# Optimization experiments

Hardware: AMD Instinct MI355X
Metric: run time of the kernel (lower is better)

The kernel has to match this reference:

```python
import jax, jax.numpy as jnp
import numpy as np


def setup_inputs() -> dict:
    key = jax.random.key(0)
    k1, k2, k3, k4, k5, k6 = jax.random.split(key, 6)
    B, V = 128, 128000
    logits = jax.random.normal(k1, (B, V), dtype=jnp.float32) * 2.0
    # keep temperatures away from 0 to avoid overflow in logits/temp
    temperatures = 0.7 + 0.6 * jax.random.uniform(k2, (B,), dtype=jnp.float32)
    top_ks = jax.random.randint(k3, (B,), 1, 1024, dtype=jnp.int32)
    top_ps = 0.7 + 0.29 * jax.random.uniform(k4, (B,), dtype=jnp.float32)
    min_ps = 0.02 * jax.random.uniform(k5, (B,), dtype=jnp.float32)
    # uniform variate for inverse-CDF multinomial sampling (one sample per row)
    u = jax.random.uniform(k6, (B, 1), dtype=jnp.float32)
    return {
        "logits": logits,
        "temperatures": temperatures,
        "top_ks": top_ks,
        "top_ps": top_ps,
        "min_ps": min_ps,
        "u": u,
    }


def reference(logits, temperatures, top_ks, top_ps, min_ps, u):
    """Faithful jax version of Sampler's torch-native sampling path:
    softmax(logits/T) -> descending sort -> top-k mask -> top-p mask
    (cumsum computed pre-mask, exactly as torch code) -> min-p mask ->
    multinomial sample (inverse CDF with provided uniform u) ->
    gather original token index. Also returns the renormalized filtered
    probs scattered back to vocab order (top_p_normalize_probs-style)."""
    B, V = logits.shape
    probs = jax.nn.softmax(logits / temperatures[:, None], axis=-1)  # [B, V]

    order = jnp.argsort(-probs, axis=-1)                     # descending indices
    probs_sort = jnp.take_along_axis(probs, order, axis=-1)  # [B, V] sorted desc
    probs_sum = jnp.cumsum(probs_sort, axis=-1)              # cumsum BEFORE masking

    pos = jnp.arange(V, dtype=jnp.int32)[None, :]
    # top-k: zero everything at rank >= top_k
    probs_sort = jnp.where(pos >= top_ks[:, None], 0.0, probs_sort)
    # top-p: zero where cumulative mass strictly before this token exceeds top_p
    probs_sort = jnp.where(probs_sum - probs_sort > top_ps[:, None], 0.0, probs_sort)
    # min-p: threshold relative to the max prob (rank-0 entry survives both masks)
    min_p_thr = probs_sort[:, :1] * min_ps[:, None]
    probs_sort = jnp.where(probs_sort < min_p_thr, 0.0, probs_sort)

    total = jnp.sum(probs_sort, axis=-1, keepdims=True)      # [B, 1]
    cdf = jnp.cumsum(probs_sort, axis=-1) / total            # normalized CDF
    # inverse-CDF sampling == torch.multinomial(probs_sort, 1)
    sampled_rank = jnp.clip(jnp.sum(cdf < u, axis=-1, keepdims=True), 0, V - 1)
    token_ids = jnp.take_along_axis(order, sampled_rank, axis=-1)[:, 0].astype(jnp.int32)

    # scatter renormalized filtered probs back to original vocab positions
    inv_order = jnp.argsort(order, axis=-1)
    norm_probs = jnp.take_along_axis(probs_sort / total, inv_order, axis=-1)
    return token_ids, norm_probs
```

## Files before the change

### kernel.cpp

```cpp
#include <hip/hip_runtime.h>
#include <stdint.h>
#include <math.h>

#define TPB 1024
#define NB 2048
#define SPLIT 4
#define LCAND 2560
#define CAND2 2048
#define PS 4096
#define L2E 1.44269504088896f

typedef float vfloat4 __attribute__((ext_vector_type(4)));
typedef unsigned long long ull;

__device__ __forceinline__ unsigned fkey(float f) {
    unsigned u = __float_as_uint(f);
    return (u & 0x80000000u) ? ~u : (u | 0x80000000u);
}
__device__ __forceinline__ float funkey(unsigned k) {
    unsigned u = (k & 0x80000000u) ? (k ^ 0x80000000u) : ~k;
    return __uint_as_float(u);
}
__device__ __forceinline__ ull packkv(unsigned k, unsigned idx) {
    return ((ull)k << 32) | (ull)(~idx);
}

__device__ __forceinline__ void suffix_scan_2048(unsigned* h, unsigned* wscr, int tid)
{
    const int lane = tid & 63, w = tid >> 6;
    const int i0 = 2047 - 2 * tid;
    const int i1 = 2046 - 2 * tid;
    unsigned a = h[i0], b = h[i1];
    unsigned s = a + b;
    unsigned inc = s;
    #pragma unroll
    for (int d = 1; d < 64; d <<= 1) { unsigned o = __shfl_up(inc, d); if (lane >= d) inc += o; }
    if (lane == 63) wscr[w] = inc;
    __syncthreads();
    if (w == 0) {
        unsigned v = (lane < 16) ? wscr[lane] : 0u;
        unsigned vi = v;
        #pragma unroll
        for (int d = 1; d < 16; d <<= 1) { unsigned o = __shfl_up(vi, d); if (lane >= d) vi += o; }
        if (lane < 16) wscr[16 + lane] = vi - v;
    }
    __syncthreads();
    unsigned off = wscr[16 + w] + (inc - s);
    h[i0] = off + a;
    h[i1] = off + a + b;
    __syncthreads();
}

__global__ __launch_bounds__(TPB)
void k1_scan(const float* __restrict__ logits,
             const float* __restrict__ temps,
             const int* __restrict__ top_ks,
             float* __restrict__ out_probs,
             float* __restrict__ ws_meta,
             unsigned* __restrict__ ws_cut,
             unsigned* __restrict__ ws_cnt,
             ull* __restrict__ ws_cand,
             int V, int Vq, int n)
{
    const int blk = blockIdx.x;
    const int tid = threadIdx.x, lane = tid & 63, w = tid >> 6;
    const int role = blk % 3;

    if (role != 0) {
        const int ZB = (gridDim.x / 3) * 2;
        const int zid = (blk / 3) * 2 + (role - 1);
        const int n4 = n >> 2;
        vfloat4* p4 = (vfloat4*)out_probs;
        const vfloat4 z4 = (vfloat4)0.0f;
        const int step = ZB * TPB;
        for (int i = zid * TPB + tid; i < n4; i += step) p4[i] = z4;
        for (int i = (n4 << 2) + zid * TPB + tid; i < n; i += step) out_probs[i] = 0.0f;
        return;
    }

    const int sblk = blk / 3;
    const int b = sblk / SPLIT, s = sblk % SPLIT;
    const int start = s * Vq;
    const int len = min(Vq, V - start);
    const int slot = sblk;
    const float invT = 1.0f / temps[b];
    int K = top_ks[b]; K = max(K, 1); K = min(K, 1024);

    __shared__ unsigned hist[NB];
    __shared__ unsigned uscr[32];
    __shared__ float fred[32];
    __shared__ unsigned cnt;
    __shared__ int bstar;

    if (len <= 0) {
        if (tid == 0) {
            ws_meta[4*slot] = -1e30f; ws_meta[4*slot+1] = 0.0f;
            ws_meta[4*slot+2] = -1e30f; ws_meta[4*slot+3] = __uint_as_float(0u);
            ws_cut[slot] = 0u; ws_cnt[slot] = 0u;
        }
        return;
    }

    for (int i = tid; i < NB; i += TPB) hist[i] = 0;
    if (tid == 0) { cnt = 0; bstar = 0; }
    __syncthreads();

    const float* __restrict__ row = logits + (size_t)b * V + start;
    const vfloat4* __restrict__ row4 = (const vfloat4*)row;
    const int L4 = len >> 2;

    const int nps = min(len, PS);
    float m0 = -1e30f;
    for (int i = tid; i < nps; i += TPB) {
        float lv = row[i];
        m0 = fmaxf(m0, lv);
        atomicAdd(&hist[fkey(lv) >> 21], 1u);
    }
    #pragma unroll
    for (int d = 32; d > 0; d >>= 1) m0 = fmaxf(m0, __shfl_down(m0, d));
    if (lane == 0) fred[w] = m0;
    __syncthreads();
    if (tid == 0) {
        float mm = fred[0];
        for (int j = 1; j < 16; ++j) mm = fmaxf(mm, fred[j]);
        fred[16] = mm;
    }
    __syncthreads();
    const float m0max = fred[16];

    suffix_scan_2048(hist, uscr, tid);
    float sexp = (float)K * (float)nps / (float)V;
    unsigned TGT = (unsigned)(sexp + 6.0f * sqrtf(sexp) + 16.5f);
    if (TGT > (unsigned)nps) TGT = (unsigned)nps;
    for (int e = tid; e < NB; e += TPB) {
        unsigned Se = hist[e];
        unsigned Sn = (e < NB - 1) ? hist[e + 1] : 0u;
        if (Se >= TGT && Sn < TGT) bstar = e;
    }
    __syncthreads();
    const unsigned cutkey = (unsigned)bstar << 21;
    const float cutval = funkey(cutkey);

    const float ca = invT * L2E;
    const float cb = -m0max * invT * L2E;

    float z = 0.0f, mb = -1e30f;
    ull* gc = ws_cand + (size_t)slot * LCAND;

    for (int i = tid; i < L4; i += TPB) {
        vfloat4 v = row4[i];
        float x0 = v[0], x1 = v[1], x2 = v[2], x3 = v[3];
        z += exp2f(fmaf(x0, ca, cb)) + exp2f(fmaf(x1, ca, cb))
           + exp2f(fmaf(x2, ca, cb)) + exp2f(fmaf(x3, ca, cb));
        mb = fmaxf(mb, fmaxf(fmaxf(x0, x1), fmaxf(x2, x3)));
        bool c0 = x0 >= cutval, c1 = x1 >= cutval, c2 = x2 >= cutval, c3 = x3 >= cutval;
        if (c0 | c1 | c2 | c3) {
            int nh = (int)c0 + (int)c1 + (int)c2 + (int)c3;
            unsigned base = atomicAdd(&cnt, (unsigned)nh);
            unsigned bi = (unsigned)(start + (i << 2));
            if (c0) { if (base < LCAND) gc[base] = packkv(fkey(x0), bi + 0); base++; }
            if (c1) { if (base < LCAND) gc[base] = packkv(fkey(x1), bi + 1); base++; }
            if (c2) { if (base < LCAND) gc[base] = packkv(fkey(x2), bi + 2); base++; }
            if (c3) { if (base < LCAND) gc[base] = packkv(fkey(x3), bi + 3); base++; }
        }
    }
    for (int i = (L4 << 2) + tid; i < len; i += TPB) {
        float lv = row[i];
        z += exp2f(fmaf(lv, ca, cb));
        mb = fmaxf(mb, lv);
        if (lv >= cutval) {
            unsigned base = atomicAdd(&cnt, 1u);
            if (base < LCAND) gc[base] = packkv(fkey(lv), (unsigned)(start + i));
        }
    }
    __syncthreads();
    #pragma unroll
    for (int d = 32; d > 0; d >>= 1) {
        z += __shfl_down(z, d);
        mb = fmaxf(mb, __shfl_down(mb, d));
    }
    if (lane == 0) { fred[w] = z; fred[16 + w] = mb; }
    __syncthreads();
    if (tid == 0) {
        float zz = 0.0f, mm = -1e30f;
        for (int j = 0; j < 16; ++j) { zz += fred[j]; mm = fmaxf(mm, fred[16 + j]); }
        ws_meta[4*slot + 0] = m0max * invT;
        ws_meta[4*slot + 1] = zz;
        ws_meta[4*slot + 2] = mm * invT;
        ws_meta[4*slot + 3] = __uint_as_float(fkey(mm));
        ws_cut[slot] = cutkey;
        ws_cnt[slot] = cnt;
    }
}

__global__ __launch_bounds__(TPB)
void k2_sample(const float* __restrict__ logits,
               const float* __restrict__ temps,
               const int* __restrict__ top_ks,
               const float* __restrict__ top_ps,
               const float* __restrict__ min_ps,
               const float* __restrict__ uvec,
               const float* __restrict__ ws_meta,
               const unsigned* __restrict__ ws_cut,
               const unsigned* __restrict__ ws_cnt,
               const ull* __restrict__ ws_cand,
               float* __restrict__ out_tok,
               float* __restrict__ out_probs,
               int V)
{
    const int b = blockIdx.x;
    const int tid = threadIdx.x, lane = tid & 63, w = tid >> 6;
    const float invT = 1.0f / temps[b];
    int Korig = top_ks[b]; Korig = max(Korig, 1); Korig = min(Korig, 1024);
    const unsigned Ku = (unsigned)Korig;
    const float top_p = top_ps[b], min_p = min_ps[b], uval = uvec[b];

    __shared__ __align__(16) char smem[53504];
    ull*            cand  = (ull*)(smem);
    ull*            cand2 = (ull*)(smem + 16384);
    unsigned*       hist  = (unsigned*)(smem + 32768);
    unsigned short* cnts  = (unsigned short*)(smem + 41216);
    float*          sh_p  = (float*)(smem + 45312);
    float*          sh_c  = (float*)(smem + 49408);
    __shared__ unsigned uscr[32];
    __shared__ float fws[32];
    __shared__ unsigned scnt;
    __shared__ int sh_i1, sh_i2;
    __shared__ unsigned sh_u1;

    float Cy[SPLIT], zq[SPLIT], Mbyq[SPLIT];
    unsigned cutq[SPLIT], cntq[SPLIT], mkq[SPLIT];
    #pragma unroll
    for (int q = 0; q < SPLIT; ++q) {
        int sl = b * SPLIT + q;
        Cy[q] = ws_meta[4*sl]; zq[q] = ws_meta[4*sl+1]; Mbyq[q] = ws_meta[4*sl+2];
        mkq[q] = __float_as_uint(ws_meta[4*sl+3]);
        cutq[q] = ws_cut[sl]; cntq[q] = ws_cnt[sl];
    }
    float Y = -1e30f;
    #pragma unroll
    for (int q = 0; q < SPLIT; ++q) Y = fmaxf(Y, Cy[q]);
    float Z = 0.0f;
    #pragma unroll
    for (int q = 0; q < SPLIT; ++q)
        if (zq[q] > 0.0f) Z += zq[q] * exp2f((Cy[q] - Y) * L2E);

    bool fb = false;
    unsigned cutmax = 0, mincut = 0xFFFFFFFFu, maxkey = 0;
    #pragma unroll
    for (int q = 0; q < SPLIT; ++q) {
        if (cntq[q] > (unsigned)LCAND) fb = true;
        if (cntq[q] > 0u) {
            if (Mbyq[q] - Cy[q] > 60.0f) fb = true;
            cutmax = max(cutmax, cutq[q]);
            mincut = min(mincut, cutq[q]);
            maxkey = max(maxkey, mkq[q]);
        }
    }
    if (mincut == 0xFFFFFFFFu) fb = true;

    const unsigned base = mincut;
    const unsigned range = maxkey - base;
    int shift = 0;
    while ((range >> shift) > (unsigned)(NB - 1)) shift++;

    unsigned Tkeyb = 0;
    int count = 0, bstar = 0;

    if (!fb) {
        for (int i = tid; i <= NB; i += TPB) hist[i] = 0;
        if (tid == 0) { sh_i1 = -1; scnt = 0; }
        __syncthreads();
        #pragma unroll
        for (int q = 0; q < SPLIT; ++q) {
            const ull* gc = ws_cand + (size_t)(b * SPLIT + q) * LCAND;
            int nl = min((int)cntq[q], LCAND);
            for (int i = tid; i < nl; i += TPB)
                atomicAdd(&hist[((unsigned)(gc[i] >> 32) - base) >> shift], 1u);
        }
        __syncthreads();
        unsigned fat = 0;
        for (int i = tid; i < NB; i += TPB) {
            unsigned h = hist[i];
            cnts[i] = (unsigned short)h;
            fat = max(fat, h);
        }
        #pragma unroll
        for (int d = 32; d > 0; d >>= 1) fat = max(fat, __shfl_down(fat, d));
        if (lane == 0) uscr[w] = fat;
        __syncthreads();
        if (tid == 0) {
            unsigned m2 = 0;
            for (int j = 0; j < 16; ++j) m2 = max(m2, uscr[j]);
            uscr[16] = m2;
        }
        __syncthreads();
        if (uscr[16] > 64u) fb = true;
    }
    if (!fb) {
        suffix_scan_2048(hist, uscr, tid);
        for (int e = tid; e < NB; e += TPB) {
            unsigned Se = hist[e], Sn = (e < NB - 1) ? hist[e + 1] : 0u;
            if (Se >= Ku && Sn < Ku) { sh_i1 = e; sh_u1 = Se; }
        }
        __syncthreads();
        if (sh_i1 < 0) fb = true;
        else {
            bstar = sh_i1;
            count = (int)sh_u1;
            Tkeyb = base + ((unsigned)bstar << shift);
            if (Tkeyb < cutmax || count > CAND2) fb = true;
        }
    }
    if (!fb) {
        #pragma unroll
        for (int q = 0; q < SPLIT; ++q) {
            const ull* gc = ws_cand + (size_t)(b * SPLIT + q) * LCAND;
            int nl = min((int)cntq[q], LCAND);
            for (int i = tid; i < nl; i += TPB) {
                ull e = gc[i];
                unsigned k = (unsigned)(e >> 32);
                if (k >= Tkeyb) {
                    unsigned bin = (k - base) >> shift;
                    unsigned pos = atomicAdd(&hist[bin + 1], 1u);
                    cand2[pos] = e;
                }
            }
        }
        __syncthreads();
        for (int e = bstar + tid; e < NB; e += TPB) {
            int c = (int)cnts[e];
            if (c >= 2) {
                int st = (int)hist[e + 1] - c;
                for (int x = 1; x < c; ++x) {
                    ull key = cand2[st + x];
                    int y = x - 1;
                    while (y >= 0 && cand2[st + y] < key) { cand2[st + y + 1] = cand2[st + y]; --y; }
                    cand2[st + y + 1] = key;
                }
            }
        }
        __syncthreads();
    }

    if (fb) {
        const float* __restrict__ row = logits + (size_t)b * V;
        float m = -1e30f, z = 0.0f;
        for (int i = tid; i < V; i += TPB) {
            float y = row[i] * invT;
            float nm = fmaxf(m, y);
            z = z * exp2f((m - nm) * L2E) + exp2f((y - nm) * L2E);
            m = nm;
        }
        sh_p[tid] = m; sh_c[tid] = z;
        __syncthreads();
        for (int d = TPB >> 1; d > 0; d >>= 1) {
            if (tid < d) {
                float m1 = sh_p[tid], z1 = sh_c[tid];
                float m2 = sh_p[tid + d], z2 = sh_c[tid + d];
                float mm = fmaxf(m1, m2);
                sh_c[tid] = z1 * exp2f((m1 - mm) * L2E) + z2 * exp2f((m2 - mm) * L2E);
                sh_p[tid] = mm;
            }
            __syncthreads();
        }
        Y = sh_p[0]; Z = sh_c[0];
        __syncthreads();
        for (int i = tid; i < NB; i += TPB) hist[i] = 0;
        if (tid == 0) { sh_i1 = 0; sh_i2 = 0; sh_u1 = 0; }
        __syncthreads();
        for (int i = tid; i < V; i += TPB) atomicAdd(&hist[fkey(row[i]) >> 21], 1u);
        __syncthreads();
        suffix_scan_2048(hist, uscr, tid);
        for (int e = tid; e < NB; e += TPB) {
            unsigned Se = hist[e], Sn = (e < NB-1) ? hist[e+1] : 0u;
            if (Se >= Ku && Sn < Ku) { sh_i1 = e; sh_u1 = Sn; }
        }
        __syncthreads();
        int b1 = sh_i1;
        unsigned cab = sh_u1;
        for (int i = tid; i < NB; i += TPB) hist[i] = 0;
        __syncthreads();
        for (int i = tid; i < V; i += TPB) {
            unsigned k = fkey(row[i]);
            if ((int)(k >> 21) == b1) atomicAdd(&hist[(k >> 10) & (NB - 1)], 1u);
        }
        __syncthreads();
        suffix_scan_2048(hist, uscr, tid);
        for (int e = tid; e < NB; e += TPB) {
            unsigned Se = cab + hist[e];
            unsigned Sn = cab + ((e < NB-1) ? hist[e+1] : 0u);
            if (Se >= Ku && Sn < Ku) sh_i2 = e;
        }
        __syncthreads();
        unsigned Tkey = ((unsigned)b1 << 21) | ((unsigned)sh_i2 << 10);
        if (tid == 0) scnt = 0;
        __syncthreads();
        for (int i = tid; i < V; i += TPB) {
            unsigned k = fkey(row[i]);
            if (k >= Tkey) {
                unsigned pos = atomicAdd(&scnt, 1u);
                if (pos < CAND2) cand[pos] = packkv(k, (unsigned)i);
            }
        }
        __syncthreads();
        count = (scnt < (unsigned)CAND2) ? (int)scnt : CAND2;

        int n_sort = 1;
        while (n_sort < count) n_sort <<= 1;
        for (int i = tid; i < n_sort; i += TPB)
            if (i >= count) cand[i] = 0ull;
        __syncthreads();
        for (int kk = 2; kk <= n_sort; kk <<= 1) {
            for (int j = kk >> 1; j > 0; j >>= 1) {
                for (int i = tid; i < n_sort; i += TPB) {
                    int ixj = i ^ j;
                    if (ixj > i) {
                        ull a = cand[i], c = cand[ixj];
                        bool up = (i & kk) == 0;
                        if (up ? (a < c) : (a > c)) { cand[i] = c; cand[ixj] = a; }
                    }
                }
                __syncthreads();
            }
        }
    }

    ull* srt = fb ? cand : cand2;
    int K = min(Korig, count);

    float pv = 0.0f;
    if (tid < K) {
        unsigned k = (unsigned)(srt[tid] >> 32);
        pv = exp2f((funkey(k) * invT - Y) * L2E) / Z;
    }
    float inc = pv;
    #pragma unroll
    for (int d = 1; d < 64; d <<= 1) { float o = __shfl_up(inc, d); if (lane >= d) inc += o; }
    if (lane == 63) fws[w] = inc;
    __syncthreads();
    if (w == 0) {
        float v = (lane < 16) ? fws[lane] : 0.0f;
        float vi = v;
        #pragma unroll
        for (int d = 1; d < 16; d <<= 1) { float o = __shfl_up(vi, d); if (lane >= d) vi += o; }
        if (lane < 16) fws[16 + lane] = vi - v;
    }
    __syncthreads();
    float cum = inc + fws[16 + w];
    sh_p[tid] = pv;
    sh_c[tid] = cum;
    if (tid == 0) sh_i1 = K;
    __syncthreads();

    if (tid < K) {
        float excl = cum - pv;
        if (excl > top_p) atomicMin(&sh_i1, tid);
    }
    __syncthreads();
    int n1 = sh_i1;
    float thr = sh_p[0] * min_p;
    if (tid == 0) sh_i2 = n1;
    __syncthreads();
    if (tid < n1 && sh_p[tid] < thr) atomicMin(&sh_i2, tid);
    __syncthreads();
    int nf = sh_i2;
    float total = sh_c[nf - 1];

    int pred = (tid < nf) && ((sh_c[tid] / total) < uval);
    int rank = __syncthreads_count(pred);
    if (rank > nf - 1) rank = nf - 1;
    if (rank < 0) rank = 0;
    if (tid == 0)
        out_tok[b] = (float)(~(unsigned)(srt[rank] & 0xFFFFFFFFull));

    if (tid < nf) {
        unsigned idx = ~(unsigned)(srt[tid] & 0xFFFFFFFFull);
        out_probs[(size_t)b * V + idx] = sh_p[tid] / total;
    }
}

extern "C" void kernel_launch(void* const* d_in, const int* in_sizes, int n_in,
                              void* d_out, int out_size, void* d_ws, size_t ws_size,
                              hipStream_t stream) {
    const float* logits = (const float*)d_in[0];
    const float* temps  = (const float*)d_in[1];
    const int*   top_ks = (const int*)d_in[2];
    const float* top_ps = (const float*)d_in[3];
    const float* min_ps = (const float*)d_in[4];
    const float* u      = (const float*)d_in[5];
    const int B = in_sizes[1];
    const int V = in_sizes[0] / B;
    float* out_tok   = (float*)d_out;
    float* out_probs = out_tok + B;

    int Vq = (((V + SPLIT - 1) / SPLIT) + 3) & ~3;
    int n = B * V;

    char* ws = (char*)d_ws;
    size_t off = 0;
    auto take = [&](size_t bytes) { char* p = ws + off; off = (off + bytes + 255) & ~(size_t)255; return p; };
    float*    ws_meta = (float*)take((size_t)B * SPLIT * 4 * sizeof(float));
    unsigned* ws_cut  = (unsigned*)take((size_t)B * SPLIT * sizeof(unsigned));
    unsigned* ws_cnt  = (unsigned*)take((size_t)B * SPLIT * sizeof(unsigned));
    ull*      ws_cand = (ull*)take((size_t)B * SPLIT * LCAND * sizeof(ull));
    (void)ws_size;

    k1_scan<<<dim3(3 * SPLIT * B), dim3(TPB), 0, stream>>>(
        logits, temps, top_ks, out_probs, ws_meta, ws_cut, ws_cnt, ws_cand, V, Vq, n);
    k2_sample<<<dim3(B), dim3(TPB), 0, stream>>>(
        logits, temps, top_ks, top_ps, min_ps, u, ws_meta, ws_cut, ws_cnt, ws_cand,
        out_tok, out_probs, V);
}
```

Measured before the change: 155.5 us.

## Fuse output zeroing into scan blocks, unroll main loop, compute max key from candidates

Removes the separate zero-filling block roles from k1 and has each scan block zero its own slice of the output with nontemporal stores, shrinking the grid threefold. The main pass over the logits is unrolled by four with independent partial sums. The per-slice running max is dropped from that loop; k2 instead recomputes the max key by scanning the candidate lists. The fallback test changes from a max-minus-prefix-max bound to finiteness checks on Z. This trades more parallel blocks for less loop overhead per element, and moves some reduction work into k2.

```diff
diff --git a/kernel.cpp b/kernel.cpp
--- a/kernel.cpp
+++ b/kernel.cpp
@@ -60,26 +60,11 @@
              unsigned* __restrict__ ws_cut,
              unsigned* __restrict__ ws_cnt,
              ull* __restrict__ ws_cand,
-             int V, int Vq, int n)
+             int V, int Vq)
 {
-    const int blk = blockIdx.x;
+    const int sblk = blockIdx.x;
+    const int b = sblk / SPLIT, s = sblk % SPLIT;
     const int tid = threadIdx.x, lane = tid & 63, w = tid >> 6;
-    const int role = blk % 3;
-
-    if (role != 0) {
-        const int ZB = (gridDim.x / 3) * 2;
-        const int zid = (blk / 3) * 2 + (role - 1);
-        const int n4 = n >> 2;
-        vfloat4* p4 = (vfloat4*)out_probs;
-        const vfloat4 z4 = (vfloat4)0.0f;
-        const int step = ZB * TPB;
-        for (int i = zid * TPB + tid; i < n4; i += step) p4[i] = z4;
-        for (int i = (n4 << 2) + zid * TPB + tid; i < n; i += step) out_probs[i] = 0.0f;
-        return;
-    }
-
-    const int sblk = blk / 3;
-    const int b = sblk / SPLIT, s = sblk % SPLIT;
     const int start = s * Vq;
     const int len = min(Vq, V - start);
     const int slot = sblk;
@@ -94,9 +79,8 @@
 
     if (len <= 0) {
         if (tid == 0) {
-            ws_meta[4*slot] = -1e30f; ws_meta[4*slot+1] = 0.0f;
-            ws_meta[4*slot+2] = -1e30f; ws_meta[4*slot+3] = __uint_as_float(0u);
-            ws_cut[slot] = 0u; ws_cnt[slot] = 0u;
+            ws_meta[2*slot] = -1e30f; ws_meta[2*slot+1] = 0.0f;
+            ws_cut[slot] = 0xFFFFFFFFu; ws_cnt[slot] = 0u;
         }
         return;
     }
@@ -141,53 +125,72 @@
     const unsigned cutkey = (unsigned)bstar << 21;
     const float cutval = funkey(cutkey);
 
+    {
+        float* __restrict__ orow = out_probs + (size_t)b * V + start;
+        vfloat4* __restrict__ orow4 = (vfloat4*)orow;
+        const vfloat4 z4 = (vfloat4)0.0f;
+        for (int i = tid; i < L4; i += TPB) __builtin_nontemporal_store(z4, &orow4[i]);
+        for (int i = (L4 << 2) + tid; i < len; i += TPB) __builtin_nontemporal_store(0.0f, &orow[i]);
+    }
+
     const float ca = invT * L2E;
     const float cb = -m0max * invT * L2E;
-
-    float z = 0.0f, mb = -1e30f;
     ull* gc = ws_cand + (size_t)slot * LCAND;
 
-    for (int i = tid; i < L4; i += TPB) {
+    float z0 = 0.0f, z1 = 0.0f, z2 = 0.0f, z3 = 0.0f;
+
+    #define E4(v) (exp2f(fmaf((v)[0], ca, cb)) + exp2f(fmaf((v)[1], ca, cb)) \
+                 + exp2f(fmaf((v)[2], ca, cb)) + exp2f(fmaf((v)[3], ca, cb)))
+    #define GATHER(v, ii) do {                                                  \
+        bool c0 = (v)[0] >= cutval, c1 = (v)[1] >= cutval,                      \
+             c2 = (v)[2] >= cutval, c3 = (v)[3] >= cutval;                      \
+        if (c0 | c1 | c2 | c3) {                                                \
+            int nh = (int)c0 + (int)c1 + (int)c2 + (int)c3;                     \
+            unsigned base = atomicAdd(&cnt, (unsigned)nh);                      \
+            unsigned bi = (unsigned)(start + ((ii) << 2));                      \
+            if (c0) { if (base < LCAND) gc[base] = packkv(fkey((v)[0]), bi+0); base++; } \
+            if (c1) { if (base < LCAND) gc[base] = packkv(fkey((v)[1]), bi+1); base++; } \
+            if (c2) { if (base < LCAND) gc[base] = packkv(fkey((v)[2]), bi+2); base++; } \
+            if (c3) { if (base < LCAND) gc[base] = packkv(fkey((v)[3]), bi+3); base++; } \
+        }                                                                       \
+    } while (0)
+
+    int i = tid;
+    for (; i + 3 * TPB < L4; i += 4 * TPB) {
+        vfloat4 va = row4[i];
+        vfloat4 vb = row4[i + TPB];
+        vfloat4 vc = row4[i + 2 * TPB];
+        vfloat4 vd = row4[i + 3 * TPB];
+        z0 += E4(va); z1 += E4(vb); z2 += E4(vc); z3 += E4(vd);
+        GATHER(va, i); GATHER(vb, i + TPB); GATHER(vc, i + 2 * TPB); GATHER(vd, i + 3 * TPB);
+    }
+    for (; i < L4; i += TPB) {
         vfloat4 v = row4[i];
-        float x0 = v[0], x1 = v[1], x2 = v[2], x3 = v[3];
-        z += exp2f(fmaf(x0, ca, cb)) + exp2f(fmaf(x1, ca, cb))
-           + exp2f(fmaf(x2, ca, cb)) + exp2f(fmaf(x3, ca, cb));
-        mb = fmaxf(mb, fmaxf(fmaxf(x0, x1), fmaxf(x2, x3)));
-        bool c0 = x0 >= cutval, c1 = x1 >= cutval, c2 = x2 >= cutval, c3 = x3 >= cutval;
-        if (c0 | c1 | c2 | c3) {
-            int nh = (int)c0 + (int)c1 + (int)c2 + (int)c3;
-            unsigned base = atomicAdd(&cnt, (unsigned)nh);
-            unsigned bi = (unsigned)(start + (i << 2));
-            if (c0) { if (base < LCAND) gc[base] = packkv(fkey(x0), bi + 0); base++; }
-            if (c1) { if (base < LCAND) gc[base] = packkv(fkey(x1), bi + 1); base++; }
-            if (c2) { if (base < LCAND) gc[base] = packkv(fkey(x2), bi + 2); base++; }
-            if (c3) { if (base < LCAND) gc[base] = packkv(fkey(x3), bi + 3); base++; }
-        }
-    }
-    for (int i = (L4 << 2) + tid; i < len; i += TPB) {
-        float lv = row[i];
-        z += exp2f(fmaf(lv, ca, cb));
-        mb = fmaxf(mb, lv);
+        z0 += E4(v);
+        GATHER(v, i);
+    }
+    for (int j = (L4 << 2) + tid; j < len; j += TPB) {
+        float lv = row[j];
+        z0 += exp2f(fmaf(lv, ca, cb));
         if (lv >= cutval) {
             unsigned base = atomicAdd(&cnt, 1u);
-            if (base < LCAND) gc[base] = packkv(fkey(lv), (unsigned)(start + i));
-        }
-    }
-    __syncthreads();
-    #pragma unroll
-    for (int d = 32; d > 0; d >>= 1) {
-        z += __shfl_down(z, d);
-        mb = fmaxf(mb, __shfl_down(mb, d));
-    }
-    if (lane == 0) { fred[w] = z; fred[16 + w] = mb; }
+            if (base < LCAND) gc[base] = packkv(fkey(lv), (unsigned)(start + j));
+        }
+    }
+    #undef E4
+    #undef GATHER
+
+    float z = (z0 + z1) + (z2 + z3);
+    __syncthreads();
+    #pragma unroll
+    for (int d = 32; d > 0; d >>= 1) z += __shfl_down(z, d);
+    if (lane == 0) fred[w] = z;
     __syncthreads();
     if (tid == 0) {
-        float zz = 0.0f, mm = -1e30f;
-        for (int j = 0; j < 16; ++j) { zz += fred[j]; mm = fmaxf(mm, fred[16 + j]); }
-        ws_meta[4*slot + 0] = m0max * invT;
-        ws_meta[4*slot + 1] = zz;
-        ws_meta[4*slot + 2] = mm * invT;
-        ws_meta[4*slot + 3] = __uint_as_float(fkey(mm));
+        float zz = 0.0f;
+        for (int j = 0; j < 16; ++j) zz += fred[j];
+        ws_meta[2*slot + 0] = m0max * invT;
+        ws_meta[2*slot + 1] = zz;
         ws_cut[slot] = cutkey;
         ws_cnt[slot] = cnt;
     }
@@ -224,53 +227,64 @@
     float*          sh_c  = (float*)(smem + 49408);
     __shared__ unsigned uscr[32];
     __shared__ float fws[32];
-    __shared__ unsigned scnt;
+    __shared__ unsigned scnt, sh_mk;
     __shared__ int sh_i1, sh_i2;
     __shared__ unsigned sh_u1;
 
-    float Cy[SPLIT], zq[SPLIT], Mbyq[SPLIT];
-    unsigned cutq[SPLIT], cntq[SPLIT], mkq[SPLIT];
+    float Cy[SPLIT], zq[SPLIT];
+    unsigned cutq[SPLIT], cntq[SPLIT];
     #pragma unroll
     for (int q = 0; q < SPLIT; ++q) {
         int sl = b * SPLIT + q;
-        Cy[q] = ws_meta[4*sl]; zq[q] = ws_meta[4*sl+1]; Mbyq[q] = ws_meta[4*sl+2];
-        mkq[q] = __float_as_uint(ws_meta[4*sl+3]);
+        Cy[q] = ws_meta[2*sl]; zq[q] = ws_meta[2*sl+1];
         cutq[q] = ws_cut[sl]; cntq[q] = ws_cnt[sl];
     }
     float Y = -1e30f;
     #pragma unroll
-    for (int q = 0; q < SPLIT; ++q) Y = fmaxf(Y, Cy[q]);
+    for (int q = 0; q < SPLIT; ++q) if (cntq[q] > 0u) Y = fmaxf(Y, Cy[q]);
     float Z = 0.0f;
     #pragma unroll
     for (int q = 0; q < SPLIT; ++q)
-        if (zq[q] > 0.0f) Z += zq[q] * exp2f((Cy[q] - Y) * L2E);
+        if (cntq[q] > 0u && zq[q] > 0.0f) Z += zq[q] * exp2f((Cy[q] - Y) * L2E);
 
     bool fb = false;
-    unsigned cutmax = 0, mincut = 0xFFFFFFFFu, maxkey = 0;
+    unsigned cutmax = 0, mincut = 0xFFFFFFFFu;
     #pragma unroll
     for (int q = 0; q < SPLIT; ++q) {
         if (cntq[q] > (unsigned)LCAND) fb = true;
         if (cntq[q] > 0u) {
-            if (Mbyq[q] - Cy[q] > 60.0f) fb = true;
+            if (!isfinite(zq[q])) fb = true;
             cutmax = max(cutmax, cutq[q]);
             mincut = min(mincut, cutq[q]);
-            maxkey = max(maxkey, mkq[q]);
-        }
-    }
-    if (mincut == 0xFFFFFFFFu) fb = true;
-
-    const unsigned base = mincut;
-    const unsigned range = maxkey - base;
-    int shift = 0;
-    while ((range >> shift) > (unsigned)(NB - 1)) shift++;
+        }
+    }
+    if (mincut == 0xFFFFFFFFu || !isfinite(Z) || Z <= 0.0f) fb = true;
 
     unsigned Tkeyb = 0;
-    int count = 0, bstar = 0;
+    int count = 0, bstar = 0, shift = 0;
+    unsigned base = mincut;
 
     if (!fb) {
+        unsigned mk = 0;
+        if (tid == 0) sh_mk = 0;
         for (int i = tid; i <= NB; i += TPB) hist[i] = 0;
         if (tid == 0) { sh_i1 = -1; scnt = 0; }
         __syncthreads();
+        #pragma unroll
+        for (int q = 0; q < SPLIT; ++q) {
+            const ull* gc = ws_cand + (size_t)(b * SPLIT + q) * LCAND;
+            int nl = min((int)cntq[q], LCAND);
+            for (int i = tid; i < nl; i += TPB)
+                mk = max(mk, (unsigned)(gc[i] >> 32));
+        }
+        #pragma unroll
+        for (int d = 32; d > 0; d >>= 1) mk = max(mk, __shfl_down(mk, d));
+        if (lane == 0) atomicMax(&sh_mk, mk);
+        __syncthreads();
+        const unsigned maxkey = sh_mk;
+        const unsigned range = maxkey - base;
+        while ((range >> shift) > (unsigned)(NB - 1)) shift++;
+
         #pragma unroll
         for (int q = 0; q < SPLIT; ++q) {
             const ull* gc = ws_cand + (size_t)(b * SPLIT + q) * LCAND;
@@ -495,19 +509,18 @@
     float* out_probs = out_tok + B;
 
     int Vq = (((V + SPLIT - 1) / SPLIT) + 3) & ~3;
-    int n = B * V;
 
     char* ws = (char*)d_ws;
     size_t off = 0;
     auto take = [&](size_t bytes) { char* p = ws + off; off = (off + bytes + 255) & ~(size_t)255; return p; };
-    float*    ws_meta = (float*)take((size_t)B * SPLIT * 4 * sizeof(float));
+    float*    ws_meta = (float*)take((size_t)B * SPLIT * 2 * sizeof(float));
     unsigned* ws_cut  = (unsigned*)take((size_t)B * SPLIT * sizeof(unsigned));
     unsigned* ws_cnt  = (unsigned*)take((size_t)B * SPLIT * sizeof(unsigned));
     ull*      ws_cand = (ull*)take((size_t)B * SPLIT * LCAND * sizeof(ull));
     (void)ws_size;
 
-    k1_scan<<<dim3(3 * SPLIT * B), dim3(TPB), 0, stream>>>(
-        logits, temps, top_ks, out_probs, ws_meta, ws_cut, ws_cnt, ws_cand, V, Vq, n);
+    k1_scan<<<dim3(SPLIT * B), dim3(TPB), 0, stream>>>(
+        logits, temps, top_ks, out_probs, ws_meta, ws_cut, ws_cnt, ws_cand, V, Vq);
     k2_sample<<<dim3(B), dim3(TPB), 0, stream>>>(
         logits, temps, top_ks, top_ps, min_ps, u, ws_meta, ws_cut, ws_cnt, ws_cand,
         out_tok, out_probs, V);
```

Result: no change. 152.5 us (-1.9%).
